# Kernel optimization log

Measured on AMD Instinct MI355X. Metric: run time of the kernel, lower is better.

The kernel has to match this reference:

```python
import jax, jax.numpy as jnp
import numpy as np

WS = (14, 14)
NUM_HEADS = 12
DIM = 768
HEAD_DIM = DIM // NUM_HEADS
N_TOK = WS[0] * WS[1] + 1  # 197 (cls token)
NUM_REL = (2 * WS[0] - 1) * (2 * WS[1] - 1) + 3  # 732
B = 64


def _build_rel_pos_index():
    ch, cw = np.arange(WS[0]), np.arange(WS[1])
    coords = np.stack(np.meshgrid(ch, cw, indexing='ij'))  # [2,h,w]
    cf = coords.reshape(2, -1)  # [2, h*w]
    rel = cf[:, :, None] - cf[:, None, :]  # [2, hw, hw]
    rel = rel.transpose(1, 2, 0).astype(np.int64)
    rel[:, :, 0] += WS[0] - 1
    rel[:, :, 1] += WS[1] - 1
    rel[:, :, 0] *= 2 * WS[1] - 1
    idx = np.zeros((N_TOK, N_TOK), dtype=np.int64)
    idx[1:, 1:] = rel.sum(-1)
    idx[0, 0:] = NUM_REL - 3
    idx[0:, 0] = NUM_REL - 2
    idx[0, 0] = NUM_REL - 1
    return idx.astype(np.int32)


def setup_inputs() -> dict:
    key = jax.random.key(0)
    ks = jax.random.split(key, 7)
    s = 0.02
    return {
        'x': jax.random.normal(ks[0], (B, N_TOK, DIM), jnp.float32),
        'qkv_w': jax.random.normal(ks[1], (3 * DIM, DIM), jnp.float32) * s,
        'q_bias': jax.random.normal(ks[2], (DIM,), jnp.float32) * s,
        'v_bias': jax.random.normal(ks[3], (DIM,), jnp.float32) * s,
        'rpb_table': jax.random.normal(ks[4], (NUM_REL, NUM_HEADS), jnp.float32) * s,
        'proj_w': jax.random.normal(ks[5], (DIM, DIM), jnp.float32) * s,
        'proj_b': jax.random.normal(ks[6], (DIM,), jnp.float32) * s,
        'rel_pos_index': jnp.asarray(_build_rel_pos_index()),
    }


def reference(x, qkv_w, q_bias, v_bias, rpb_table, proj_w, proj_b, rel_pos_index):
    Bb, N, C = x.shape
    scale = HEAD_DIM ** -0.5
    # qkv bias: [q_bias, zeros(k), v_bias]
    qkv_bias = jnp.concatenate([q_bias, jnp.zeros_like(v_bias), v_bias])
    qkv = x @ qkv_w.T + qkv_bias  # [B,N,3C]
    qkv = qkv.reshape(Bb, N, 3, NUM_HEADS, HEAD_DIM).transpose(2, 0, 3, 1, 4)
    q, k, v = qkv[0], qkv[1], qkv[2]  # [B,H,N,hd]
    attn = jnp.einsum('bhnd,bhmd->bhnm', q * scale, k)
    # gather relative position bias: [N,N,H] -> [1,H,N,N]
    rpb = rpb_table[rel_pos_index]  # [N,N,H]
    attn = attn + rpb.transpose(2, 0, 1)[None]
    attn = jax.nn.softmax(attn, axis=-1)
    out = jnp.einsum('bhnm,bhmd->bhnd', attn, v)
    out = out.transpose(0, 2, 1, 3).reshape(Bb, N, NUM_HEADS * HEAD_DIM)
    return out @ proj_w.T + proj_b
```

## Files before the change

### kernel.cpp

```cpp
#include <hip/hip_runtime.h>
#include <hip/hip_bf16.h>
#include <cstdint>
#include <cstddef>

typedef __bf16 bf16x8 __attribute__((ext_vector_type(8)));
typedef float f32x4 __attribute__((ext_vector_type(4)));

#define DI __device__ __forceinline__

DI unsigned short f2bf(float x) {
    union { float f; unsigned int u; } v; v.f = x;
    unsigned int u = v.u;
    u += 0x7FFFu + ((u >> 16) & 1u);
    return (unsigned short)(u >> 16);
}

#define BATCH 64
#define NH 12
#define NTOK 197
#define NTOK_P 208
#define HD 64
#define DIM 768
#define MROWS 12608
#define MPAD 224
#define PLDS 232
#define CPAD 132

DI int xcd_swz(int orig, int nwg) {
    int q = nwg >> 3, r = nwg & 7;
    int x = orig & 7, l = orig >> 3;
    return (x < r ? x * (q + 1) : r * (q + 1) + (x - r) * q) + l;
}


__global__ void cvt_bf16_kernel(const float* __restrict__ in, unsigned short* __restrict__ out, int n4) {
    int i = blockIdx.x * blockDim.x + threadIdx.x;
    if (i >= n4) return;
    float4 f = ((const float4*)in)[i];
    ushort4 o;
    o.x = f2bf(f.x); o.y = f2bf(f.y); o.z = f2bf(f.z); o.w = f2bf(f.w);
    ((ushort4*)out)[i] = o;
}

__global__ void build_rpb_kernel(const float* __restrict__ table, const int* __restrict__ idx,
                                 float* __restrict__ out) {
    int i = blockIdx.x * blockDim.x + threadIdx.x;
    if (i >= NH * NTOK_P * NTOK_P) return;
    int r = i % NTOK_P; int c = (i / NTOK_P) % NTOK_P; int h = i / (NTOK_P * NTOK_P);
    float v = 0.f;
    if (r < NTOK && c < NTOK) v = table[idx[r * NTOK + c] * NH + h];
    out[i] = v;
}

__global__ void zero_vt_pad_kernel(unsigned short* __restrict__ vt) {
    const int npad = MPAD - NTOK;
    int i = blockIdx.x * blockDim.x + threadIdx.x;
    if (i >= BATCH * NH * HD * npad) return;
    int c = NTOK + (i % npad);
    int row = i / npad;
    vt[(size_t)row * MPAD + c] = 0;
}


DI int swz(int row, int col_elem) {
    return (row * 64 + col_elem) ^ ((row & 7) << 3);
}

template<int EPI>
__launch_bounds__(256)
__global__ void gemm_bt_kernel(const unsigned short* __restrict__ A,
                               const unsigned short* __restrict__ W,
                               const float* __restrict__ bias0,
                               const float* __restrict__ bias1,
                               void* __restrict__ out0,
                               unsigned short* __restrict__ out1,
                               unsigned short* __restrict__ out2,
                               int M, int ntiles)
{
    __shared__ __align__(16) unsigned short smem[32768];
    const int K = DIM;
    const int NT = K / 64;
    int wgid = xcd_swz(blockIdx.x, gridDim.x);
    int mt = wgid / ntiles, nt = wgid % ntiles;
    int m0 = mt * 128, n0 = nt * 128;
    int tid = threadIdx.x;
    int lane = tid & 63, w = tid >> 6;
    int wr = (w >> 1) * 64, wc = (w & 1) * 64;

    const int st_row = lane >> 3;
    const int st_col = ((lane & 7) ^ (lane >> 3)) << 3;

    f32x4 acc[4][4] = {};

    auto stage = [&](int buf, int ks) {
        unsigned short* as = smem + buf * 8192;
        unsigned short* bs = smem + 16384 + buf * 8192;
#pragma unroll
        for (int i = 0; i < 4; i++) {
            int s = w * 4 + i;
            int arow = m0 + s * 8 + st_row; if (arow >= M) arow = M - 1;
            __builtin_amdgcn_global_load_lds(
                (const __attribute__((address_space(1))) void*)(A + (size_t)arow * K + ks + st_col),
                (__attribute__((address_space(3))) void*)(as + s * 512), 16, 0, 0);
        }
#pragma unroll
        for (int i = 0; i < 4; i++) {
            int s = w * 4 + i;
            __builtin_amdgcn_global_load_lds(
                (const __attribute__((address_space(1))) void*)(W + (size_t)(n0 + s * 8 + st_row) * K + ks + st_col),
                (__attribute__((address_space(3))) void*)(bs + s * 512), 16, 0, 0);
        }
    };

    stage(0, 0);
    __syncthreads();
    int cur = 0;
    for (int t = 0; t < NT; ++t) {
        if (t + 1 < NT) stage(cur ^ 1, (t + 1) * 64);
        const unsigned short* as = smem + cur * 8192;
        const unsigned short* bs = smem + 16384 + cur * 8192;
#pragma unroll
        for (int kc = 0; kc < 2; kc++) {
            bf16x8 af[4], bfr[4];
#pragma unroll
            for (int x = 0; x < 4; x++)
                af[x] = *(const bf16x8*)&as[swz(wr + x * 16 + (lane & 15), kc * 32 + (lane >> 4) * 8)];
#pragma unroll
            for (int y = 0; y < 4; y++)
                bfr[y] = *(const bf16x8*)&bs[swz(wc + y * 16 + (lane & 15), kc * 32 + (lane >> 4) * 8)];
#pragma unroll
            for (int x = 0; x < 4; x++)
#pragma unroll
                for (int y = 0; y < 4; y++)
                    acc[x][y] = __builtin_amdgcn_mfma_f32_16x16x32_bf16(af[x], bfr[y], acc[x][y], 0, 0, 0);
        }
        __syncthreads();
        cur ^= 1;
    }

    if constexpr (EPI == 1) {
#pragma unroll
        for (int x = 0; x < 4; x++)
#pragma unroll
            for (int y = 0; y < 4; y++)
#pragma unroll
                for (int j = 0; j < 4; j++) {
                    int m = m0 + wr + x * 16 + (lane >> 4) * 4 + j;
                    int n = n0 + wc + y * 16 + (lane & 15);
                    if (m < M)
                        ((float*)out0)[(size_t)m * DIM + n] = acc[x][y][j] + bias0[n];
                }
    } else {
        int which = n0 / DIM;
        int hn0 = n0 - which * DIM;
        unsigned short* lc = smem;

#pragma unroll
        for (int x = 0; x < 4; x++)
#pragma unroll
            for (int y = 0; y < 4; y++)
#pragma unroll
                for (int j = 0; j < 4; j++) {
                    int ml = wr + x * 16 + (lane >> 4) * 4 + j;
                    int nl = wc + y * 16 + (lane & 15);
                    float val = acc[x][y][j];
                    if (which == 0) val = (val + bias0[hn0 + nl]) * 0.125f;
                    else if (which == 2) val = val + bias1[hn0 + nl];
                    lc[ml * CPAD + nl] = f2bf(val);
                }
        __syncthreads();

        if (which != 2) {
            unsigned short* outq = (which == 0) ? (unsigned short*)out0 : out1;
            int c4 = (lane & 31) * 4;
            int h = (hn0 >> 6) + (c4 >> 6), d = c4 & 63;
            for (int it = 0; it < 16; ++it) {
                int r = it * 8 + w * 2 + (lane >> 5);
                int m = m0 + r;
                if (m >= M) continue;
                int b = m / NTOK, t = m - b * NTOK;
                ushort4 q4 = *(const ushort4*)&lc[r * CPAD + c4];
                *(ushort4*)&outq[(((size_t)b * NH + h) * NTOK_P + t) * HD + d] = q4;
            }
        } else {
            int mh = w >> 1, hs = w & 1;
            int h = (hn0 >> 6) + hs;
            int ml = mh * 64 + lane;
            int m = m0 + ml;
            if (m < M) {
                int b = m / NTOK, t = m - b * NTOK;
                unsigned short* vbase = out2 + (((size_t)b * NH + h) * HD) * MPAD + t;
#pragma unroll 8
                for (int d = 0; d < 64; ++d)
                    vbase[(size_t)d * MPAD] = lc[ml * CPAD + hs * 64 + d];
            }
        }
    }
}


__launch_bounds__(64)
__global__ void attn_kernel(const unsigned short* __restrict__ qbuf,
                            const unsigned short* __restrict__ kbuf,
                            const unsigned short* __restrict__ vt,
                            const float* __restrict__ rpbT,
                            unsigned short* __restrict__ ao)
{
    __shared__ __align__(16) unsigned short p_lds[16][PLDS];
    int bid = xcd_swz(blockIdx.x, gridDim.x);
    int qt = bid % 13, bh = bid / 13;
    int b = bh / NH, h = bh - b * NH;
    int lane = threadIdx.x;
    int r0 = qt * 16;

    {
        int rr = lane >> 2, cc = NTOK_P + (lane & 3) * 4;
        ushort4 z = {0, 0, 0, 0};
        *(ushort4*)&p_lds[rr][cc] = z;
    }

    const size_t kqbase = (size_t)bh * NTOK_P * HD;
    int qrow = r0 + (lane & 15);
    bf16x8 qf0 = *(const bf16x8*)&qbuf[kqbase + (size_t)qrow * HD + (lane >> 4) * 8];
    bf16x8 qf1 = *(const bf16x8*)&qbuf[kqbase + (size_t)qrow * HD + 32 + (lane >> 4) * 8];

    f32x4 s[13];
#pragma unroll
    for (int t = 0; t < 13; t++) {
        int krow = t * 16 + (lane & 15);
        bf16x8 kf0 = *(const bf16x8*)&kbuf[kqbase + (size_t)krow * HD + (lane >> 4) * 8];
        bf16x8 kf1 = *(const bf16x8*)&kbuf[kqbase + (size_t)krow * HD + 32 + (lane >> 4) * 8];
        f32x4 z = {0.f, 0.f, 0.f, 0.f};
        f32x4 a = __builtin_amdgcn_mfma_f32_16x16x32_bf16(qf0, kf0, z, 0, 0, 0);
        s[t] = __builtin_amdgcn_mfma_f32_16x16x32_bf16(qf1, kf1, a, 0, 0, 0);
    }

    int col_l = lane & 15;
    int rbase = r0 + (lane >> 4) * 4;
    float mrow[4] = {-1e30f, -1e30f, -1e30f, -1e30f};
#pragma unroll
    for (int t = 0; t < 13; t++) {
        int col = t * 16 + col_l;
        bool masked = (col >= NTOK);
        float4 rb = *(const float4*)&rpbT[((size_t)h * NTOK_P + col) * NTOK_P + rbase];
        float rbj[4] = {rb.x, rb.y, rb.z, rb.w};
#pragma unroll
        for (int j = 0; j < 4; j++) {
            float v = s[t][j] + rbj[j];
            if (masked) v = -1e30f;
            s[t][j] = v;
            mrow[j] = fmaxf(mrow[j], v);
        }
    }
#pragma unroll
    for (int j = 0; j < 4; j++) {
        float mv = mrow[j];
        mv = fmaxf(mv, __shfl_xor(mv, 1));
        mv = fmaxf(mv, __shfl_xor(mv, 2));
        mv = fmaxf(mv, __shfl_xor(mv, 4));
        mv = fmaxf(mv, __shfl_xor(mv, 8));
        mrow[j] = mv;
    }
    float lrow[4] = {0.f, 0.f, 0.f, 0.f};
#pragma unroll
    for (int t = 0; t < 13; t++)
#pragma unroll
        for (int j = 0; j < 4; j++) {
            float p = __expf(s[t][j] - mrow[j]);
            s[t][j] = p;
            lrow[j] += p;
        }
#pragma unroll
    for (int j = 0; j < 4; j++) {
        float lv = lrow[j];
        lv += __shfl_xor(lv, 1);
        lv += __shfl_xor(lv, 2);
        lv += __shfl_xor(lv, 4);
        lv += __shfl_xor(lv, 8);
        lrow[j] = lv;
    }
#pragma unroll
    for (int t = 0; t < 13; t++)
#pragma unroll
        for (int j = 0; j < 4; j++)
            p_lds[(lane >> 4) * 4 + j][t * 16 + col_l] = f2bf(s[t][j]);

    f32x4 o[4] = {};
    const size_t vbase = (size_t)bh * HD * MPAD;
#pragma unroll
    for (int c = 0; c < 7; c++) {
        bf16x8 pf = *(const bf16x8*)&p_lds[lane & 15][c * 32 + (lane >> 4) * 8];
#pragma unroll
        for (int n = 0; n < 4; n++) {
            bf16x8 vf = *(const bf16x8*)&vt[vbase + (size_t)(n * 16 + (lane & 15)) * MPAD + c * 32 + (lane >> 4) * 8];
            o[n] = __builtin_amdgcn_mfma_f32_16x16x32_bf16(pf, vf, o[n], 0, 0, 0);
        }
    }
#pragma unroll
    for (int n = 0; n < 4; n++)
#pragma unroll
        for (int j = 0; j < 4; j++) {
            int tok = rbase + j;
            if (tok < NTOK) {
                float val = o[n][j] / lrow[j];
                ao[((size_t)b * NTOK + tok) * DIM + h * HD + n * 16 + col_l] = f2bf(val);
            }
        }
}


extern "C" void kernel_launch(void* const* d_in, const int* in_sizes, int n_in,
                              void* d_out, int out_size, void* d_ws, size_t ws_size,
                              hipStream_t stream)
{
    const float* x      = (const float*)d_in[0];
    const float* qkv_w  = (const float*)d_in[1];
    const float* q_bias = (const float*)d_in[2];
    const float* v_bias = (const float*)d_in[3];
    const float* rpb_t  = (const float*)d_in[4];
    const float* proj_w = (const float*)d_in[5];
    const float* proj_b = (const float*)d_in[6];
    const int*   relidx = (const int*)d_in[7];
    float* out = (float*)d_out;

    char* ws = (char*)d_ws;
    const size_t SZ_XBF  = (size_t)MROWS * DIM * 2;
    const size_t SZ_QKVW = (size_t)3 * DIM * DIM * 2;
    const size_t SZ_PRJW = (size_t)DIM * DIM * 2;
    const size_t SZ_QK   = (size_t)BATCH * NH * NTOK_P * HD * 2;
    const size_t SZ_VT   = (size_t)BATCH * NH * HD * MPAD * 2;

    unsigned short* x_bf = (unsigned short*)ws;
    unsigned short* ao   = x_bf;
    size_t off = SZ_XBF;
    unsigned short* qkvw_bf  = (unsigned short*)(ws + off); off += SZ_QKVW;
    unsigned short* projw_bf = (unsigned short*)(ws + off); off += SZ_PRJW;
    unsigned short* qbuf     = (unsigned short*)(ws + off); off += SZ_QK;
    unsigned short* kbuf     = (unsigned short*)(ws + off); off += SZ_QK;
    unsigned short* vtbuf    = (unsigned short*)(ws + off); off += SZ_VT;
    float* rpbf              = (float*)(ws + off);

    cvt_bf16_kernel<<<(MROWS * DIM / 4 + 255) / 256, 256, 0, stream>>>(x, x_bf, MROWS * DIM / 4);
    cvt_bf16_kernel<<<(3 * DIM * DIM / 4 + 255) / 256, 256, 0, stream>>>(qkv_w, qkvw_bf, 3 * DIM * DIM / 4);
    cvt_bf16_kernel<<<(DIM * DIM / 4 + 255) / 256, 256, 0, stream>>>(proj_w, projw_bf, DIM * DIM / 4);
    build_rpb_kernel<<<(NH * NTOK_P * NTOK_P + 255) / 256, 256, 0, stream>>>(rpb_t, relidx, rpbf);
    zero_vt_pad_kernel<<<(BATCH * NH * HD * (MPAD - NTOK) + 255) / 256, 256, 0, stream>>>(vtbuf);

    gemm_bt_kernel<0><<<99 * 18, 256, 0, stream>>>(x_bf, qkvw_bf, q_bias, v_bias,
                                                   (void*)qbuf, kbuf, vtbuf, MROWS, 18);
    attn_kernel<<<BATCH * NH * 13, 64, 0, stream>>>(qbuf, kbuf, vtbuf, rpbf, ao);
    gemm_bt_kernel<1><<<99 * 6, 256, 0, stream>>>(ao, projw_bf, proj_b, nullptr,
                                                  (void*)out, nullptr, nullptr, MROWS, 6);
    (void)in_sizes; (void)n_in; (void)out_size; (void)ws_size;
}
```

Baseline: 207.5 us.

## Fuse bf16 conversions, relayout rel-pos bias per lane, use exp2 softmax

Merges the three fp32-to-bf16 conversion launches into one kernel. Rebuilds the relative position bias in a per-lane, per-tile order premultiplied by log2(e) so each attention lane reads it contiguously, and folds log2(e) into the Q scale so softmax can use exp2f. Also replaces the per-element division with a reciprocal multiply and raises wave priority around the MFMA loops. Each piece targets a small cost (launch overhead, scattered bias loads, exp and divide latency), at the price of slightly different rounding from the fast reciprocal.

New measurement: 212.6 us. +2.5%, slower.

```diff
diff --git a/kernel.cpp b/kernel.cpp
--- a/kernel.cpp
+++ b/kernel.cpp
@@ -7,6 +7,8 @@
 typedef float f32x4 __attribute__((ext_vector_type(4)));
 
 #define DI __device__ __forceinline__
+#define AS1 __attribute__((address_space(1)))
+#define AS3 __attribute__((address_space(3)))
 
 DI unsigned short f2bf(float x) {
     union { float f; unsigned int u; } v; v.f = x;
@@ -25,6 +27,8 @@
 #define MPAD 224
 #define PLDS 232
 #define CPAD 132
+#define QSCALE 0.18033688f
+#define LOG2E 1.4426950408889634f
 
 DI int xcd_swz(int orig, int nwg) {
     int q = nwg >> 3, r = nwg & 7;
@@ -32,23 +36,39 @@
     return (x < r ? x * (q + 1) : r * (q + 1) + (x - r) * q) + l;
 }
 
-
-__global__ void cvt_bf16_kernel(const float* __restrict__ in, unsigned short* __restrict__ out, int n4) {
+DI int swz(int row, int col_elem) {
+    return (row * 64 + col_elem) ^ ((row & 7) << 3);
+}
+
+
+__global__ void cvt3_bf16_kernel(const float* __restrict__ a, unsigned short* __restrict__ oa, int na4,
+                                 const float* __restrict__ b, unsigned short* __restrict__ ob, int nb4,
+                                 const float* __restrict__ c, unsigned short* __restrict__ oc, int nc4) {
     int i = blockIdx.x * blockDim.x + threadIdx.x;
-    if (i >= n4) return;
-    float4 f = ((const float4*)in)[i];
+    const float* src; unsigned short* dst; int k;
+    if (i < na4) { src = a; dst = oa; k = i; }
+    else if (i < na4 + nb4) { src = b; dst = ob; k = i - na4; }
+    else if (i < na4 + nb4 + nc4) { src = c; dst = oc; k = i - na4 - nb4; }
+    else return;
+    float4 f = ((const float4*)src)[k];
     ushort4 o;
     o.x = f2bf(f.x); o.y = f2bf(f.y); o.z = f2bf(f.z); o.w = f2bf(f.w);
-    ((ushort4*)out)[i] = o;
-}
-
-__global__ void build_rpb_kernel(const float* __restrict__ table, const int* __restrict__ idx,
-                                 float* __restrict__ out) {
+    ((ushort4*)dst)[k] = o;
+}
+
+__global__ void build_rpb2_kernel(const float* __restrict__ table, const int* __restrict__ idx,
+                                  float* __restrict__ out) {
     int i = blockIdx.x * blockDim.x + threadIdx.x;
-    if (i >= NH * NTOK_P * NTOK_P) return;
-    int r = i % NTOK_P; int c = (i / NTOK_P) % NTOK_P; int h = i / (NTOK_P * NTOK_P);
+    if (i >= NH * 13 * 13 * 256) return;
+    int j = i & 3;
+    int lane = (i >> 2) & 63;
+    int t = (i >> 8) % 13;
+    int qt = ((i >> 8) / 13) % 13;
+    int h = (i >> 8) / 169;
+    int row = qt * 16 + ((lane >> 4) << 2) + j;
+    int col = t * 16 + (lane & 15);
     float v = 0.f;
-    if (r < NTOK && c < NTOK) v = table[idx[r * NTOK + c] * NH + h];
+    if (row < NTOK && col < NTOK) v = table[idx[row * NTOK + col] * NH + h] * LOG2E;
     out[i] = v;
 }
 
@@ -61,10 +81,6 @@
     vt[(size_t)row * MPAD + c] = 0;
 }
 
-
-DI int swz(int row, int col_elem) {
-    return (row * 64 + col_elem) ^ ((row & 7) << 3);
-}
 
 template<int EPI>
 __launch_bounds__(256)
@@ -100,15 +116,15 @@
             int s = w * 4 + i;
             int arow = m0 + s * 8 + st_row; if (arow >= M) arow = M - 1;
             __builtin_amdgcn_global_load_lds(
-                (const __attribute__((address_space(1))) void*)(A + (size_t)arow * K + ks + st_col),
-                (__attribute__((address_space(3))) void*)(as + s * 512), 16, 0, 0);
+                (const AS1 void*)(A + (size_t)arow * K + ks + st_col),
+                (AS3 void*)(as + s * 512), 16, 0, 0);
         }
 #pragma unroll
         for (int i = 0; i < 4; i++) {
             int s = w * 4 + i;
             __builtin_amdgcn_global_load_lds(
-                (const __attribute__((address_space(1))) void*)(W + (size_t)(n0 + s * 8 + st_row) * K + ks + st_col),
-                (__attribute__((address_space(3))) void*)(bs + s * 512), 16, 0, 0);
+                (const AS1 void*)(W + (size_t)(n0 + s * 8 + st_row) * K + ks + st_col),
+                (AS3 void*)(bs + s * 512), 16, 0, 0);
         }
     };
 
@@ -164,7 +180,7 @@
                     int ml = wr + x * 16 + (lane >> 4) * 4 + j;
                     int nl = wc + y * 16 + (lane & 15);
                     float val = acc[x][y][j];
-                    if (which == 0) val = (val + bias0[hn0 + nl]) * 0.125f;
+                    if (which == 0) val = (val + bias0[hn0 + nl]) * QSCALE;
                     else if (which == 2) val = val + bias1[hn0 + nl];
                     lc[ml * CPAD + nl] = f2bf(val);
                 }
@@ -203,7 +219,7 @@
 __global__ void attn_kernel(const unsigned short* __restrict__ qbuf,
                             const unsigned short* __restrict__ kbuf,
                             const unsigned short* __restrict__ vt,
-                            const float* __restrict__ rpbT,
+                            const float* __restrict__ rpb2,
                             unsigned short* __restrict__ ao)
 {
     __shared__ __align__(16) unsigned short p_lds[16][PLDS];
@@ -225,6 +241,7 @@
     bf16x8 qf1 = *(const bf16x8*)&qbuf[kqbase + (size_t)qrow * HD + 32 + (lane >> 4) * 8];
 
     f32x4 s[13];
+    __builtin_amdgcn_s_setprio(1);
 #pragma unroll
     for (int t = 0; t < 13; t++) {
         int krow = t * 16 + (lane & 15);
@@ -234,15 +251,17 @@
         f32x4 a = __builtin_amdgcn_mfma_f32_16x16x32_bf16(qf0, kf0, z, 0, 0, 0);
         s[t] = __builtin_amdgcn_mfma_f32_16x16x32_bf16(qf1, kf1, a, 0, 0, 0);
     }
+    __builtin_amdgcn_s_setprio(0);
 
     int col_l = lane & 15;
     int rbase = r0 + (lane >> 4) * 4;
+    const float* rpbase = rpb2 + (((size_t)(h * 13 + qt) * 13) << 8) + (lane << 2);
     float mrow[4] = {-1e30f, -1e30f, -1e30f, -1e30f};
 #pragma unroll
     for (int t = 0; t < 13; t++) {
         int col = t * 16 + col_l;
         bool masked = (col >= NTOK);
-        float4 rb = *(const float4*)&rpbT[((size_t)h * NTOK_P + col) * NTOK_P + rbase];
+        float4 rb = *(const float4*)&rpbase[t << 8];
         float rbj[4] = {rb.x, rb.y, rb.z, rb.w};
 #pragma unroll
         for (int j = 0; j < 4; j++) {
@@ -266,7 +285,7 @@
     for (int t = 0; t < 13; t++)
 #pragma unroll
         for (int j = 0; j < 4; j++) {
-            float p = __expf(s[t][j] - mrow[j]);
+            float p = exp2f(s[t][j] - mrow[j]);
             s[t][j] = p;
             lrow[j] += p;
         }
@@ -279,6 +298,11 @@
         lv += __shfl_xor(lv, 8);
         lrow[j] = lv;
     }
+    float inv[4];
+#pragma unroll
+    for (int j = 0; j < 4; j++)
+        inv[j] = __builtin_amdgcn_rcpf(lrow[j]);
+
 #pragma unroll
     for (int t = 0; t < 13; t++)
 #pragma unroll
@@ -287,6 +311,7 @@
 
     f32x4 o[4] = {};
     const size_t vbase = (size_t)bh * HD * MPAD;
+    __builtin_amdgcn_s_setprio(1);
 #pragma unroll
     for (int c = 0; c < 7; c++) {
         bf16x8 pf = *(const bf16x8*)&p_lds[lane & 15][c * 32 + (lane >> 4) * 8];
@@ -296,13 +321,14 @@
             o[n] = __builtin_amdgcn_mfma_f32_16x16x32_bf16(pf, vf, o[n], 0, 0, 0);
         }
     }
+    __builtin_amdgcn_s_setprio(0);
 #pragma unroll
     for (int n = 0; n < 4; n++)
 #pragma unroll
         for (int j = 0; j < 4; j++) {
             int tok = rbase + j;
             if (tok < NTOK) {
-                float val = o[n][j] / lrow[j];
+                float val = o[n][j] * inv[j];
                 ao[((size_t)b * NTOK + tok) * DIM + h * HD + n * 16 + col_l] = f2bf(val);
             }
         }
@@ -340,10 +366,10 @@
     unsigned short* vtbuf    = (unsigned short*)(ws + off); off += SZ_VT;
     float* rpbf              = (float*)(ws + off);
 
-    cvt_bf16_kernel<<<(MROWS * DIM / 4 + 255) / 256, 256, 0, stream>>>(x, x_bf, MROWS * DIM / 4);
-    cvt_bf16_kernel<<<(3 * DIM * DIM / 4 + 255) / 256, 256, 0, stream>>>(qkv_w, qkvw_bf, 3 * DIM * DIM / 4);
-    cvt_bf16_kernel<<<(DIM * DIM / 4 + 255) / 256, 256, 0, stream>>>(proj_w, projw_bf, DIM * DIM / 4);
-    build_rpb_kernel<<<(NH * NTOK_P * NTOK_P + 255) / 256, 256, 0, stream>>>(rpb_t, relidx, rpbf);
+    const int NA4 = MROWS * DIM / 4, NB4 = 3 * DIM * DIM / 4, NC4 = DIM * DIM / 4;
+    cvt3_bf16_kernel<<<(NA4 + NB4 + NC4 + 255) / 256, 256, 0, stream>>>(
+        x, x_bf, NA4, qkv_w, qkvw_bf, NB4, proj_w, projw_bf, NC4);
+    build_rpb2_kernel<<<(NH * 13 * 13 * 256 + 255) / 256, 256, 0, stream>>>(rpb_t, relidx, rpbf);
     zero_vt_pad_kernel<<<(BATCH * NH * HD * (MPAD - NTOK) + 255) / 256, 256, 0, stream>>>(vtbuf);
 
     gemm_bt_kernel<0><<<99 * 18, 256, 0, stream>>>(x_bf, qkvw_bf, q_bias, v_bias,
```
